# Kernel optimization log

Hardware: AMD Instinct MI355X
Metric: run time of the kernel (lower is better)

The kernel has to match this reference:

```python
import jax, jax.numpy as jnp
import numpy as np

D_MODEL = 768
NUM_HEADS = 12
HEAD_DIM = D_MODEL // NUM_HEADS


def setup_inputs() -> dict:
    key = jax.random.key(0)
    ks = jax.random.split(key, 9)
    B, S = 2, 2048
    s = 1.0 / np.sqrt(D_MODEL)
    x = jax.random.normal(ks[0], (B, S, D_MODEL), dtype=jnp.float32)
    Wq = jax.random.normal(ks[1], (D_MODEL, D_MODEL), dtype=jnp.float32) * s
    Wk = jax.random.normal(ks[2], (D_MODEL, D_MODEL), dtype=jnp.float32) * s
    Wv = jax.random.normal(ks[3], (D_MODEL, D_MODEL), dtype=jnp.float32) * s
    Wo = jax.random.normal(ks[4], (D_MODEL, D_MODEL), dtype=jnp.float32) * s
    bq = jax.random.normal(ks[5], (D_MODEL,), dtype=jnp.float32) * 0.01
    bk = jax.random.normal(ks[6], (D_MODEL,), dtype=jnp.float32) * 0.01
    bv = jax.random.normal(ks[7], (D_MODEL,), dtype=jnp.float32) * 0.01
    bo = jax.random.normal(ks[8], (D_MODEL,), dtype=jnp.float32) * 0.01
    return {"x": x, "Wq": Wq, "bq": bq, "Wk": Wk, "bk": bk,
            "Wv": Wv, "bv": bv, "Wo": Wo, "bo": bo}


def reference(x, Wq, bq, Wk, bk, Wv, bv, Wo, bo):
    B, S, _ = x.shape
    # projections; reshape to [B, H, S, Dh]
    def split_heads(t):
        return t.reshape(B, S, NUM_HEADS, HEAD_DIM).transpose(0, 2, 1, 3)
    q = split_heads(x @ Wq + bq)
    k = split_heads(x @ Wk + bk)
    v = split_heads(x @ Wv + bv)
    scale = 1.0 / np.sqrt(HEAD_DIM)
    scores = jnp.einsum("bhqd,bhkd->bhqk", q, k) * scale  # [B,H,S,S]
    attn = jax.nn.softmax(scores, axis=-1)
    # dropout p=0.0 (eval) -> identity
    ctx = jnp.einsum("bhqk,bhkd->bhqd", attn, v)
    ctx = ctx.transpose(0, 2, 1, 3).reshape(B, S, D_MODEL)
    return ctx @ Wo + bo
```

## Files before the change

kernel.cpp:

```cpp
#include <hip/hip_runtime.h>
#include <hip/hip_bf16.h>
#include <hip/hip_fp16.h>

#define D_MODEL 768
#define NHEADS  12
#define HD      64
#define BATCH   2
#define SEQ     2048
#define NTOK    (BATCH*SEQ)
#define NX      ((size_t)NTOK * D_MODEL)
#define NW      ((size_t)D_MODEL * D_MODEL)
#define NBH     (BATCH*NHEADS)
#define SC_LOG2 0.18033688f

typedef __attribute__((ext_vector_type(8))) short    short8;
typedef __attribute__((ext_vector_type(8))) _Float16 half8;
typedef __attribute__((ext_vector_type(2))) __fp16   fp16x2;
typedef __attribute__((ext_vector_type(4))) float    f32x4;

__device__ __forceinline__ float bf2f(short s) {
    union { unsigned u; float f; } c;
    c.u = ((unsigned)(unsigned short)s) << 16;
    return c.f;
}
__device__ __forceinline__ short f2bf(float f) {
    __hip_bfloat16 h = __float2bfloat16(f);
    return *(short*)&h;
}

#ifdef __has_builtin
#if __has_builtin(__builtin_amdgcn_global_load_lds)
#define HAS_GLD 1
#endif
#if __has_builtin(__builtin_amdgcn_exp2f)
#define EXP2(x) __builtin_amdgcn_exp2f(x)
#else
#define EXP2(x) exp2f(x)
#endif
#if __has_builtin(__builtin_amdgcn_cvt_pkrtz)
#define HAS_PKRTZ 1
#endif
#else
#define EXP2(x) exp2f(x)
#endif
#ifdef HAS_GLD
#define GLD16(gp, lp) __builtin_amdgcn_global_load_lds( \
    (const __attribute__((address_space(1))) void*)(gp), \
    (__attribute__((address_space(3))) void*)(lp), 16, 0, 0)
#endif

#ifdef HAS_PKRTZ
#define PKF16(a, b) __builtin_amdgcn_cvt_pkrtz((a), (b))
#else
#define PKF16(a, b) ((fp16x2){ (__fp16)(a), (__fp16)(b) })
#endif

__global__ __launch_bounds__(256) void fused_conv(
        const void* __restrict__ xin,
        const void* __restrict__ w0, const void* __restrict__ w1,
        const void* __restrict__ w2, const void* __restrict__ w3,
        const void* __restrict__ b0, const void* __restrict__ b1,
        const void* __restrict__ b2, const void* __restrict__ b3,
        short* __restrict__ xc, short* __restrict__ wt,
        short* __restrict__ bc, int* __restrict__ flag)
{
    __shared__ int red[256];
    __shared__ float T[64][65];
    const int tid = threadIdx.x;
    const int F = blockIdx.x;

    {
        const short* xs = (const short*)xin;
        int maxe = 0;
#pragma unroll
        for (int u = 0; u < 16; ++u) {
            int e = ((unsigned short)xs[tid * 16 + u] >> 7) & 0xFF;
            maxe = max(maxe, e);
        }
        red[tid] = maxe;
        __syncthreads();
        for (int s = 128; s > 0; s >>= 1) {
            if (tid < s) red[tid] = max(red[tid], red[tid + s]);
            __syncthreads();
        }
    }
    const bool isf = (red[0] > 140);

    if (F < 3072) {
        const int i = F * 256 + tid;
        if (isf) {
            float4 f = ((const float4*)xin)[i];
            short4 o = { f2bf(f.x), f2bf(f.y), f2bf(f.z), f2bf(f.w) };
            ((short4*)xc)[i] = o;
        } else {
            ((short4*)xc)[i] = ((const short4*)xin)[i];
        }
    } else if (F < 3648) {
        const int G = F - 3072;
        const int z = G / 144, rr = G % 144;
        const int k0 = (rr % 12) * 64, n0 = (rr / 12) * 64;
        const void* src = (z == 0) ? w0 : (z == 1) ? w1 : (z == 2) ? w2 : w3;
        const float sc = (z == 0) ? SC_LOG2 : 1.0f;
        const int la = tid & 15, lb = tid >> 4;
#pragma unroll
        for (int u = 0; u < 4; ++u) {
            const int kr = (lb & 3) + 4 * u + 16 * (lb >> 2);
            if (isf) {
                float4 f = *(const float4*)((const float*)src + (size_t)(k0 + kr) * D_MODEL + n0 + la * 4);
                T[kr][la*4+0] = f.x; T[kr][la*4+1] = f.y; T[kr][la*4+2] = f.z; T[kr][la*4+3] = f.w;
            } else {
                short4 s = *(const short4*)((const short*)src + (size_t)(k0 + kr) * D_MODEL + n0 + la * 4);
                T[kr][la*4+0] = bf2f(s.x); T[kr][la*4+1] = bf2f(s.y);
                T[kr][la*4+2] = bf2f(s.z); T[kr][la*4+3] = bf2f(s.w);
            }
        }
        __syncthreads();
#pragma unroll
        for (int u = 0; u < 4; ++u) {
            const int nr = (lb & 3) + 4 * u + 16 * (lb >> 2);
            short4 o = { f2bf(T[la*4+0][nr] * sc), f2bf(T[la*4+1][nr] * sc),
                         f2bf(T[la*4+2][nr] * sc), f2bf(T[la*4+3][nr] * sc) };
            *(short4*)(wt + (size_t)z * NW + (size_t)(n0 + nr) * D_MODEL + k0 + la * 4) = o;
        }
    } else {
        if (tid == 0) *flag = isf ? 1 : 0;
        const void* srcs[4] = { b0, b1, b2, b3 };
        for (int z = 0; z < 4; ++z) {
            const float sc = (z == 0) ? SC_LOG2 : 1.0f;
            for (int i = tid; i < D_MODEL; i += 256) {
                float v = isf ? ((const float*)srcs[z])[i] : bf2f(((const short*)srcs[z])[i]);
                bc[z * D_MODEL + i] = f2bf(v * sc);
            }
        }
    }
}

__global__ __launch_bounds__(512) void qkv_gemm(const short* __restrict__ X,
                                                const short* __restrict__ Wt,
                                                const short* __restrict__ bias,
                                                short* __restrict__ qb,
                                                short* __restrict__ kb,
                                                _Float16* __restrict__ Vt)
{
    __shared__ __align__(16) char shbuf[32768];
    short* Als = (short*)shbuf;
    short* Bls = (short*)(shbuf + 16384);
    _Float16* T = (_Float16*)shbuf;

    const int tid = threadIdx.x;
    const int wave = tid >> 6, lane = tid & 63;
    const int quad = lane >> 4, l16 = lane & 15;
    const int wm = wave & 3, wn = wave >> 2;
    const int m0 = blockIdx.x * 128;
    const int ng = blockIdx.y * 128;

    f32x4 acc[2][4];
#pragma unroll
    for (int nt = 0; nt < 4; ++nt) {
        const float bv = bf2f(bias[ng + wn*64 + nt*16 + l16]);
#pragma unroll
        for (int mt = 0; mt < 2; ++mt) acc[mt][nt] = (f32x4){bv, bv, bv, bv};
    }

    const int row = tid >> 2, ch = (tid & 3) * 8;
#ifdef HAS_GLD
#define QSTAGE(buf, k0) do { \
        GLD16(X  + (size_t)(m0 + row) * D_MODEL + (k0) + ch, &Als[(buf)*4096 + tid*8]); \
        GLD16(Wt + (size_t)(ng + row) * D_MODEL + (k0) + ch, &Bls[(buf)*4096 + tid*8]); \
    } while (0)
#else
#define QSTAGE(buf, k0) do { \
        short8 r0 = *(const short8*)(X  + (size_t)(m0 + row) * D_MODEL + (k0) + ch); \
        short8 r1 = *(const short8*)(Wt + (size_t)(ng + row) * D_MODEL + (k0) + ch); \
        *(short8*)&Als[(buf)*4096 + tid*8] = r0; \
        *(short8*)&Bls[(buf)*4096 + tid*8] = r1; \
    } while (0)
#endif

    QSTAGE(0, 0);
    __syncthreads();

    for (int ks = 0; ks < 24; ++ks) {
        const int cur = ks & 1;
        if (ks + 1 < 24) QSTAGE(cur ^ 1, (ks + 1) * 32);

        short8 a[2], b[4];
#pragma unroll
        for (int mt = 0; mt < 2; ++mt)
            a[mt] = *(const short8*)&Als[cur*4096 + (wm*32 + mt*16 + l16) * 32 + quad*8];
#pragma unroll
        for (int nt = 0; nt < 4; ++nt)
            b[nt] = *(const short8*)&Bls[cur*4096 + (wn*64 + nt*16 + l16) * 32 + quad*8];
#pragma unroll
        for (int mt = 0; mt < 2; ++mt)
#pragma unroll
        for (int nt = 0; nt < 4; ++nt)
            acc[mt][nt] = __builtin_amdgcn_mfma_f32_16x16x32_bf16(a[mt], b[nt], acc[mt][nt], 0, 0, 0);

        __syncthreads();
    }
#undef QSTAGE

    const int seg = blockIdx.y / 6;
    if (seg == 0) {
#pragma unroll
        for (int mt = 0; mt < 2; ++mt)
#pragma unroll
        for (int nt = 0; nt < 4; ++nt) {
            const int n = ng + wn*64 + nt*16 + l16;
#pragma unroll
            for (int r = 0; r < 4; ++r) {
                const int m = m0 + wm*32 + mt*16 + quad*4 + r;
                qb[(size_t)m * D_MODEL + n] = f2bf(acc[mt][nt][r]);
            }
        }
    } else if (seg == 1) {
        const int nl = ng - 768;
#pragma unroll
        for (int mt = 0; mt < 2; ++mt)
#pragma unroll
        for (int nt = 0; nt < 4; ++nt) {
            const int n = nl + wn*64 + nt*16 + l16;
            const int h = n >> 6, dh = n & 63;
            const int chunk = dh >> 3, dof = dh & 7;
#pragma unroll
            for (int r = 0; r < 4; ++r) {
                const int m = m0 + wm*32 + mt*16 + quad*4 + r;
                const int b2 = m >> 11, tok = m & (SEQ - 1);
                kb[((size_t)(b2*NHEADS + h)*32 + (tok >> 6))*4096
                   + chunk*512 + (tok & 63)*8 + dof] = f2bf(acc[mt][nt][r]);
            }
        }
    } else {
        const int batch = m0 >> 11, tokb0 = m0 & (SEQ - 1);
#pragma unroll
        for (int p = 0; p < 2; ++p) {
            if ((wm >> 1) == p) {
#pragma unroll
                for (int nt = 0; nt < 4; ++nt) {
                    const int dim_l = wn*64 + nt*16 + l16;
#pragma unroll
                    for (int mt = 0; mt < 2; ++mt) {
                        const int tok_l = (wm & 1)*32 + mt*16 + quad*4;
                        union { _Float16 h4[4]; int2 v; } u;
#pragma unroll
                        for (int r = 0; r < 4; ++r) u.h4[r] = (_Float16)acc[mt][nt][r];
                        *(int2*)&T[dim_l * 72 + tok_l] = u.v;
                    }
                }
            }
            __syncthreads();
#pragma unroll
            for (int u = 0; u < 2; ++u) {
                const int slot = tid + u * 512;
                const int drow = slot & 127, chk = slot >> 7;
                int4 val = *(const int4*)&T[drow * 72 + chk * 8];
                const int dim_g = ng - 1536 + drow;
                const int h = dim_g >> 6, dl = dim_g & 63;
                *(int4*)(Vt + ((size_t)((batch*NHEADS + h)*32) + (tokb0 >> 6) + p)*4096
                            + chk*512 + dl*8) = val;
            }
            if (p == 0) __syncthreads();
        }
    }
}

__global__ __launch_bounds__(256) void out_gemm(const _Float16* __restrict__ Op,
                                                const float* __restrict__ mlp,
                                                const short* __restrict__ Wt,
                                                const short* __restrict__ bias,
                                                void* __restrict__ outv,
                                                const int* __restrict__ flag)
{
    __shared__ short Als[2][2048];
    __shared__ short Bls[2][2048];

    const int tid = threadIdx.x;
    const int wave = tid >> 6, lane = tid & 63;
    const int quad = lane >> 4, l16 = lane & 15;
    const int m0 = blockIdx.x * 64;
    const int n0 = blockIdx.y * 64;

    f32x4 acc[4];
#pragma unroll
    for (int nt = 0; nt < 4; ++nt) {
        const float bv = bf2f(bias[n0 + nt*16 + l16]);
        acc[nt] = (f32x4){bv, bv, bv, bv};
    }

    const int row = tid >> 2, ch = (tid & 3) * 8;
    const int m = m0 + row;
    const int bhb = (m >> 11) * NHEADS;
    const int qq = m & (SEQ - 1);
    const _Float16* Op2 = Op + (size_t)(NBH * SEQ) * HD;

#define MLOAD(h) do { \
        const size_t r1 = (size_t)(bhb + (h)) * SEQ + qq; \
        const float2 ml1 = *(const float2*)&mlp[r1 * 2]; \
        const float2 ml2 = *(const float2*)&mlp[((size_t)(NBH * SEQ) + r1) * 2]; \
        const float M_ = fmaxf(ml1.x, ml2.x); \
        const float w1 = EXP2(ml1.x - M_) * ml1.y; \
        const float w2 = EXP2(ml2.x - M_) * ml2.y; \
        const float s_ = 1.0f / (w1 + w2); \
        f1 = w1 * s_; f2 = w2 * s_; \
    } while (0)

#define PLOAD(ks) do { \
        const int d = ((ks) & 1) * 32 + ch; \
        const size_t r1 = (size_t)(bhb + ((ks) >> 1)) * SEQ + qq; \
        p1 = *(const half8*)&Op[r1 * HD + d]; \
        p2 = *(const half8*)&Op2[r1 * HD + d]; \
    } while (0)

#define XSTORE(buf) do { \
        short8 xb; \
        _Pragma("unroll") \
        for (int j = 0; j < 8; ++j) \
            xb[j] = f2bf(f1 * (float)p1[j] + f2 * (float)p2[j]); \
        *(short8*)&Als[buf][tid*8] = xb; \
    } while (0)

#ifdef HAS_GLD
#define BSTAGE(buf, k0) \
        GLD16(Wt + (size_t)(n0 + row) * D_MODEL + (k0) + ch, &Bls[buf][tid*8])
#else
#define BSTAGE(buf, k0) do { \
        short8 r1_ = *(const short8*)(Wt + (size_t)(n0 + row) * D_MODEL + (k0) + ch); \
        *(short8*)&Bls[buf][tid*8] = r1_; } while (0)
#endif

    half8 p1, p2; float f1, f2;
    MLOAD(0); PLOAD(0); XSTORE(0);
    BSTAGE(0, 0);
    __syncthreads();

    for (int ks = 0; ks < 24; ++ks) {
        const int cur = ks & 1;
        if (ks + 1 < 24) {
            if (((ks + 1) & 1) == 0) MLOAD((ks + 1) >> 1);
            PLOAD(ks + 1);
            BSTAGE(cur ^ 1, (ks + 1) * 32);
        }

        short8 a = *(const short8*)&Als[cur][(wave*16 + l16) * 32 + quad*8];
#pragma unroll
        for (int nt = 0; nt < 4; ++nt) {
            short8 b = *(const short8*)&Bls[cur][(nt*16 + l16) * 32 + quad*8];
            acc[nt] = __builtin_amdgcn_mfma_f32_16x16x32_bf16(a, b, acc[nt], 0, 0, 0);
        }

        if (ks + 1 < 24) XSTORE(cur ^ 1);
        __syncthreads();
    }
#undef MLOAD
#undef PLOAD
#undef XSTORE
#undef BSTAGE

    const bool outf32 = (*flag != 0);
#pragma unroll
    for (int nt = 0; nt < 4; ++nt) {
        const int n = n0 + nt*16 + l16;
#pragma unroll
        for (int r = 0; r < 4; ++r) {
            const int mm = m0 + wave*16 + quad*4 + r;
            const size_t idx = (size_t)mm * D_MODEL + n;
            if (outf32) ((float*)outv)[idx] = acc[nt][r];
            else        ((short*)outv)[idx] = f2bf(acc[nt][r]);
        }
    }
}

__global__ __launch_bounds__(256, 3) void attn_mfma(const short* __restrict__ q,
                                                    const short* __restrict__ k,
                                                    const _Float16* __restrict__ Vt,
                                                    _Float16* __restrict__ Op,
                                                    float* __restrict__ mlp)
{
    __shared__ __align__(16) short    Kls[2][4096];
    __shared__ __align__(16) _Float16 Vls[2][4096];
    __shared__ __align__(16) _Float16 Pls[4][2048];

    const int tid  = threadIdx.x;
    const int wave = tid >> 6, lane = tid & 63;
    const int quad = lane >> 4, l16 = lane & 15;

    const int F = blockIdx.x;
    const int xcd = F & 7, slot = F >> 3;
    const int bh = xcd * 3 + (slot >> 5);
    const int rem = slot & 31;
    const int q0 = (rem >> 1) * 128;
    const int sp = rem & 1;
    const int b = bh / NHEADS, h = bh % NHEADS;
    const size_t bS = (size_t)b * SEQ;

    short8 qf[2][2];
#pragma unroll
    for (int col = 0; col < 2; ++col)
#pragma unroll
    for (int k0h = 0; k0h < 2; ++k0h)
        qf[col][k0h] = *(const short8*)(q + (bS + q0 + wave*32 + col*16 + l16) * D_MODEL
                                          + h*HD + k0h*32 + quad*8);

    half8 ones;
#pragma unroll
    for (int j = 0; j < 8; ++j) ones[j] = (_Float16)1.0f;

    const short*    kbase = k  + ((size_t)bh*32 + sp*16) * 4096;
    const _Float16* vbase = Vt + ((size_t)bh*32 + sp*16) * 4096;

#ifdef HAS_GLD
#define STAGE_K(buf, j0) do { \
        GLD16(kbase + (size_t)(j0)*64 + tid*8,       &Kls[buf][tid*8]); \
        GLD16(kbase + (size_t)(j0)*64 + (tid+256)*8, &Kls[buf][(tid+256)*8]); \
    } while (0)
#define STAGE_V(buf, j0) do { \
        GLD16(vbase + (size_t)(j0)*64 + tid*8,       &Vls[buf][tid*8]); \
        GLD16(vbase + (size_t)(j0)*64 + (tid+256)*8, &Vls[buf][(tid+256)*8]); \
    } while (0)
#else
#define STAGE_K(buf, j0) do { \
        short8 a_ = *(const short8*)(kbase + (size_t)(j0)*64 + tid*8); \
        short8 b_ = *(const short8*)(kbase + (size_t)(j0)*64 + (tid+256)*8); \
        *(short8*)&Kls[buf][tid*8] = a_;  *(short8*)&Kls[buf][(tid+256)*8] = b_; \
    } while (0)
#define STAGE_V(buf, j0) do { \
        half8 c_ = *(const half8*)(vbase + (size_t)(j0)*64 + tid*8); \
        half8 d_ = *(const half8*)(vbase + (size_t)(j0)*64 + (tid+256)*8); \
        *(half8*)&Vls[buf][tid*8] = c_;  *(half8*)&Vls[buf][(tid+256)*8] = d_; \
    } while (0)
#endif

    float m_ = -1e30f;
    f32x4 laccA = (f32x4){0.f,0.f,0.f,0.f}, laccB = (f32x4){0.f,0.f,0.f,0.f};
    f32x4 o[4][2];
#pragma unroll
    for (int t = 0; t < 4; ++t) { o[t][0] = (f32x4){0.f,0.f,0.f,0.f}; o[t][1] = (f32x4){0.f,0.f,0.f,0.f}; }

#define NT (SEQ / 2 / 64)

#define QK(S, KB) do { \
    _Pragma("unroll") \
    for (int t = 0; t < 4; ++t) { S[t][0] = (f32x4){0.f,0.f,0.f,0.f}; S[t][1] = (f32x4){0.f,0.f,0.f,0.f}; } \
    _Pragma("unroll") \
    for (int k0h = 0; k0h < 2; ++k0h) \
    _Pragma("unroll") \
    for (int t = 0; t < 4; ++t) { \
        short8 kf = *(const short8*)&Kls[KB][(k0h*4 + quad)*512 + (t*16 + l16)*8]; \
        S[t][0] = __builtin_amdgcn_mfma_f32_16x16x32_bf16(kf, qf[0][k0h], S[t][0], 0, 0, 0); \
        S[t][1] = __builtin_amdgcn_mfma_f32_16x16x32_bf16(kf, qf[1][k0h], S[t][1], 0, 0, 0); \
    } \
} while (0)

#define PV(VB) do { \
    _Pragma("unroll") \
    for (int k0h = 0; k0h < 2; ++k0h) { \
        half8 pf0 = *(half8*)&Pls[wave][(k0h*4 + quad)*128 + l16*8]; \
        half8 pf1 = *(half8*)&Pls[wave][1024 + (k0h*4 + quad)*128 + l16*8]; \
        laccA = __builtin_amdgcn_mfma_f32_16x16x32_f16(ones, pf0, laccA, 0, 0, 0); \
        laccB = __builtin_amdgcn_mfma_f32_16x16x32_f16(ones, pf1, laccB, 0, 0, 0); \
        _Pragma("unroll") \
        for (int t = 0; t < 4; ++t) { \
            half8 vf = *(const half8*)&Vls[VB][(k0h*4 + quad)*512 + (t*16 + l16)*8]; \
            o[t][0] = __builtin_amdgcn_mfma_f32_16x16x32_f16(vf, pf0, o[t][0], 0, 0, 0); \
            o[t][1] = __builtin_amdgcn_mfma_f32_16x16x32_f16(vf, pf1, o[t][1], 0, 0, 0); \
        } \
    } \
} while (0)

#define SOFTMAX(S) do { \
    float mx = S[0][0][0]; \
    _Pragma("unroll") \
    for (int t = 0; t < 4; ++t) \
    _Pragma("unroll") \
    for (int c = 0; c < 2; ++c) \
    _Pragma("unroll") \
    for (int r = 0; r < 4; ++r) mx = fmaxf(mx, S[t][c][r]); \
    if (__any(mx > m_ + 8.f)) { \
        _Pragma("unroll") \
        for (int d = 1; d < 64; d <<= 1) mx = fmaxf(mx, __shfl_xor(mx, d)); \
        const float mn = fmaxf(m_, mx); \
        const float al = EXP2(m_ - mn); \
        _Pragma("unroll") \
        for (int t = 0; t < 4; ++t) \
        _Pragma("unroll") \
        for (int c = 0; c < 2; ++c) { \
            o[t][c][0] *= al; o[t][c][1] *= al; o[t][c][2] *= al; o[t][c][3] *= al; \
        } \
        laccA[0] *= al; laccB[0] *= al; \
        m_ = mn; \
    } \
    _Pragma("unroll") \
    for (int t = 0; t < 4; ++t) \
    _Pragma("unroll") \
    for (int c = 0; c < 2; ++c) { \
        union { fp16x2 h2[2]; int2 v; } u4; \
        u4.h2[0] = PKF16(EXP2(S[t][c][0] - m_), EXP2(S[t][c][1] - m_)); \
        u4.h2[1] = PKF16(EXP2(S[t][c][2] - m_), EXP2(S[t][c][3] - m_)); \
        const int kc = 2*t + (quad >> 1); \
        *(int2*)&Pls[wave][c*1024 + kc*128 + l16*8 + (quad & 1)*4] = u4.v; \
    } \
} while (0)

#define BODY(JT) do { \
    if ((JT) + 2 < NT) STAGE_K(((JT) + 2) & 1, ((JT) + 2) * 64); \
    if ((JT) + 1 < NT) STAGE_V(((JT) + 1) & 1, ((JT) + 1) * 64); \
    f32x4 s_[4][2]; \
    __builtin_amdgcn_s_setprio(1); \
    if ((JT) + 1 < NT) QK(s_, ((JT) + 1) & 1); \
    PV((JT) & 1); \
    __builtin_amdgcn_s_setprio(0); \
    if ((JT) + 1 < NT) SOFTMAX(s_); \
    __syncthreads(); \
} while (0)

    STAGE_K(0, 0); STAGE_V(0, 0);
    __syncthreads();
    STAGE_K(1, 64);
    {
        f32x4 s_[4][2];
        QK(s_, 0);
        SOFTMAX(s_);
    }
    __syncthreads();

    for (int jt = 0; jt < NT; ++jt) BODY(jt);

#pragma unroll
    for (int col = 0; col < 2; ++col) {
        const f32x4 la = col ? laccB : laccA;
        const float inv = 1.0f / la[0];
        const int myq = q0 + wave*32 + col*16 + l16;
        const size_t prow = ((size_t)sp * (NBH * SEQ) + (size_t)bh * SEQ + myq);
        _Float16* orow = Op + prow * HD;
#pragma unroll
        for (int t = 0; t < 4; ++t) {
            union { _Float16 h4[4]; int2 v; } u4;
#pragma unroll
            for (int r = 0; r < 4; ++r) u4.h4[r] = (_Float16)(o[t][col][r] * inv);
            *(int2*)(orow + t*16 + quad*4) = u4.v;
        }
        if (quad == 0) {
            float2 mlv; mlv.x = m_; mlv.y = la[0];
            *(float2*)&mlp[prow * 2] = mlv;
        }
    }
#undef BODY
#undef SOFTMAX
#undef PV
#undef QK
#undef NT
#undef STAGE_K
#undef STAGE_V
}

extern "C" void kernel_launch(void* const* d_in, const int* in_sizes, int n_in,
                              void* d_out, int out_size, void* d_ws, size_t ws_size,
                              hipStream_t stream)
{
    int* flag = (int*)d_ws;
    short* xc = (short*)((char*)d_ws + 64);
    short* Wt = xc + NX;
    short* bc = Wt + 4 * NW;
    short* qb = bc + 4 * D_MODEL;
    short* kb = qb + NX;
    _Float16* Vt = (_Float16*)(kb + NX);
    _Float16* Op = (_Float16*)(Vt + NX);
    float* mlp = (float*)(Op + (size_t)2 * NBH * SEQ * HD);

    fused_conv<<<3649, 256, 0, stream>>>(d_in[0],
                                         d_in[1], d_in[3], d_in[5], d_in[7],
                                         d_in[2], d_in[4], d_in[6], d_in[8],
                                         xc, Wt, bc, flag);

    qkv_gemm<<<dim3(NTOK/128, 2304/128), 512, 0, stream>>>(xc, Wt, bc, qb, kb, Vt);

    attn_mfma<<<768, 256, 0, stream>>>(qb, kb, Vt, Op, mlp);

    out_gemm<<<dim3(NTOK/64, D_MODEL/64), 256, 0, stream>>>(Op, mlp, Wt + 3*NW, bc + 3*D_MODEL, d_out, flag);
}
```

Measured before the change: 169.1 us.

## Split attention keys four ways and read K/V fragments directly from global

Raises the key-dimension split from 2 to 4, doubling the attention grid and raising the occupancy hint, and extends the combine step in the output GEMM to merge four partial results. It also drops the LDS double-buffered K/V staging and its per-tile barriers, loading MFMA fragments straight from global memory into registers. This aims to improve CU utilisation and remove sync overhead, but it exposes global-load latency in the inner loop and doubles the partial-output traffic and combine work.

New measurement: 195.1 us. 15.4% more time.

```diff
diff --git a/kernel.cpp b/kernel.cpp
--- a/kernel.cpp
+++ b/kernel.cpp
@@ -11,6 +11,7 @@
 #define NX      ((size_t)NTOK * D_MODEL)
 #define NW      ((size_t)D_MODEL * D_MODEL)
 #define NBH     (BATCH*NHEADS)
+#define NSPLIT  4
 #define SC_LOG2 0.18033688f
 
 typedef __attribute__((ext_vector_type(8))) short    short8;
@@ -292,31 +293,39 @@
     const int m = m0 + row;
     const int bhb = (m >> 11) * NHEADS;
     const int qq = m & (SEQ - 1);
-    const _Float16* Op2 = Op + (size_t)(NBH * SEQ) * HD;
 
 #define MLOAD(h) do { \
         const size_t r1 = (size_t)(bhb + (h)) * SEQ + qq; \
-        const float2 ml1 = *(const float2*)&mlp[r1 * 2]; \
-        const float2 ml2 = *(const float2*)&mlp[((size_t)(NBH * SEQ) + r1) * 2]; \
-        const float M_ = fmaxf(ml1.x, ml2.x); \
-        const float w1 = EXP2(ml1.x - M_) * ml1.y; \
-        const float w2 = EXP2(ml2.x - M_) * ml2.y; \
-        const float s_ = 1.0f / (w1 + w2); \
-        f1 = w1 * s_; f2 = w2 * s_; \
+        float2 ml[NSPLIT]; float M_ = -1e30f; \
+        _Pragma("unroll") \
+        for (int s = 0; s < NSPLIT; ++s) { \
+            ml[s] = *(const float2*)&mlp[((size_t)s * (NBH * SEQ) + r1) * 2]; \
+            M_ = fmaxf(M_, ml[s].x); \
+        } \
+        float w[NSPLIT]; float tot = 0.f; \
+        _Pragma("unroll") \
+        for (int s = 0; s < NSPLIT; ++s) { w[s] = EXP2(ml[s].x - M_) * ml[s].y; tot += w[s]; } \
+        const float inv_ = 1.0f / tot; \
+        _Pragma("unroll") \
+        for (int s = 0; s < NSPLIT; ++s) fw[s] = w[s] * inv_; \
     } while (0)
 
 #define PLOAD(ks) do { \
         const int d = ((ks) & 1) * 32 + ch; \
         const size_t r1 = (size_t)(bhb + ((ks) >> 1)) * SEQ + qq; \
-        p1 = *(const half8*)&Op[r1 * HD + d]; \
-        p2 = *(const half8*)&Op2[r1 * HD + d]; \
+        _Pragma("unroll") \
+        for (int s = 0; s < NSPLIT; ++s) \
+            p[s] = *(const half8*)&Op[((size_t)s * (NBH * SEQ) + r1) * HD + d]; \
     } while (0)
 
 #define XSTORE(buf) do { \
         short8 xb; \
         _Pragma("unroll") \
-        for (int j = 0; j < 8; ++j) \
-            xb[j] = f2bf(f1 * (float)p1[j] + f2 * (float)p2[j]); \
+        for (int j = 0; j < 8; ++j) { \
+            float v_ = fw[0] * (float)p[0][j] + fw[1] * (float)p[1][j] \
+                     + fw[2] * (float)p[2][j] + fw[3] * (float)p[3][j]; \
+            xb[j] = f2bf(v_); \
+        } \
         *(short8*)&Als[buf][tid*8] = xb; \
     } while (0)
 
@@ -329,7 +338,7 @@
         *(short8*)&Bls[buf][tid*8] = r1_; } while (0)
 #endif
 
-    half8 p1, p2; float f1, f2;
+    half8 p[NSPLIT]; float fw[NSPLIT];
     MLOAD(0); PLOAD(0); XSTORE(0);
     BSTAGE(0, 0);
     __syncthreads();
@@ -371,14 +380,12 @@
     }
 }
 
-__global__ __launch_bounds__(256, 3) void attn_mfma(const short* __restrict__ q,
+__global__ __launch_bounds__(256, 4) void attn_mfma(const short* __restrict__ q,
                                                     const short* __restrict__ k,
                                                     const _Float16* __restrict__ Vt,
                                                     _Float16* __restrict__ Op,
                                                     float* __restrict__ mlp)
 {
-    __shared__ __align__(16) short    Kls[2][4096];
-    __shared__ __align__(16) _Float16 Vls[2][4096];
     __shared__ __align__(16) _Float16 Pls[4][2048];
 
     const int tid  = threadIdx.x;
@@ -387,10 +394,10 @@
 
     const int F = blockIdx.x;
     const int xcd = F & 7, slot = F >> 3;
-    const int bh = xcd * 3 + (slot >> 5);
-    const int rem = slot & 31;
-    const int q0 = (rem >> 1) * 128;
-    const int sp = rem & 1;
+    const int bh = xcd * 3 + (slot >> 6);
+    const int rem = slot & 63;
+    const int q0 = (rem >> 2) * 128;
+    const int sp = rem & 3;
     const int b = bh / NHEADS, h = bh % NHEADS;
     const size_t bS = (size_t)b * SEQ;
 
@@ -406,30 +413,8 @@
 #pragma unroll
     for (int j = 0; j < 8; ++j) ones[j] = (_Float16)1.0f;
 
-    const short*    kbase = k  + ((size_t)bh*32 + sp*16) * 4096;
-    const _Float16* vbase = Vt + ((size_t)bh*32 + sp*16) * 4096;
-
-#ifdef HAS_GLD
-#define STAGE_K(buf, j0) do { \
-        GLD16(kbase + (size_t)(j0)*64 + tid*8,       &Kls[buf][tid*8]); \
-        GLD16(kbase + (size_t)(j0)*64 + (tid+256)*8, &Kls[buf][(tid+256)*8]); \
-    } while (0)
-#define STAGE_V(buf, j0) do { \
-        GLD16(vbase + (size_t)(j0)*64 + tid*8,       &Vls[buf][tid*8]); \
-        GLD16(vbase + (size_t)(j0)*64 + (tid+256)*8, &Vls[buf][(tid+256)*8]); \
-    } while (0)
-#else
-#define STAGE_K(buf, j0) do { \
-        short8 a_ = *(const short8*)(kbase + (size_t)(j0)*64 + tid*8); \
-        short8 b_ = *(const short8*)(kbase + (size_t)(j0)*64 + (tid+256)*8); \
-        *(short8*)&Kls[buf][tid*8] = a_;  *(short8*)&Kls[buf][(tid+256)*8] = b_; \
-    } while (0)
-#define STAGE_V(buf, j0) do { \
-        half8 c_ = *(const half8*)(vbase + (size_t)(j0)*64 + tid*8); \
-        half8 d_ = *(const half8*)(vbase + (size_t)(j0)*64 + (tid+256)*8); \
-        *(half8*)&Vls[buf][tid*8] = c_;  *(half8*)&Vls[buf][(tid+256)*8] = d_; \
-    } while (0)
-#endif
+    const short*    kT = k  + ((size_t)bh*32 + sp*8) * 4096 + quad*512 + l16*8;
+    const _Float16* vT = Vt + ((size_t)bh*32 + sp*8) * 4096 + quad*512 + l16*8;
 
     float m_ = -1e30f;
     f32x4 laccA = (f32x4){0.f,0.f,0.f,0.f}, laccB = (f32x4){0.f,0.f,0.f,0.f};
@@ -437,94 +422,78 @@
 #pragma unroll
     for (int t = 0; t < 4; ++t) { o[t][0] = (f32x4){0.f,0.f,0.f,0.f}; o[t][1] = (f32x4){0.f,0.f,0.f,0.f}; }
 
-#define NT (SEQ / 2 / 64)
-
-#define QK(S, KB) do { \
-    _Pragma("unroll") \
-    for (int t = 0; t < 4; ++t) { S[t][0] = (f32x4){0.f,0.f,0.f,0.f}; S[t][1] = (f32x4){0.f,0.f,0.f,0.f}; } \
-    _Pragma("unroll") \
-    for (int k0h = 0; k0h < 2; ++k0h) \
-    _Pragma("unroll") \
-    for (int t = 0; t < 4; ++t) { \
-        short8 kf = *(const short8*)&Kls[KB][(k0h*4 + quad)*512 + (t*16 + l16)*8]; \
-        S[t][0] = __builtin_amdgcn_mfma_f32_16x16x32_bf16(kf, qf[0][k0h], S[t][0], 0, 0, 0); \
-        S[t][1] = __builtin_amdgcn_mfma_f32_16x16x32_bf16(kf, qf[1][k0h], S[t][1], 0, 0, 0); \
-    } \
-} while (0)
-
-#define PV(VB) do { \
-    _Pragma("unroll") \
-    for (int k0h = 0; k0h < 2; ++k0h) { \
-        half8 pf0 = *(half8*)&Pls[wave][(k0h*4 + quad)*128 + l16*8]; \
-        half8 pf1 = *(half8*)&Pls[wave][1024 + (k0h*4 + quad)*128 + l16*8]; \
-        laccA = __builtin_amdgcn_mfma_f32_16x16x32_f16(ones, pf0, laccA, 0, 0, 0); \
-        laccB = __builtin_amdgcn_mfma_f32_16x16x32_f16(ones, pf1, laccB, 0, 0, 0); \
-        _Pragma("unroll") \
-        for (int t = 0; t < 4; ++t) { \
-            half8 vf = *(const half8*)&Vls[VB][(k0h*4 + quad)*512 + (t*16 + l16)*8]; \
-            o[t][0] = __builtin_amdgcn_mfma_f32_16x16x32_f16(vf, pf0, o[t][0], 0, 0, 0); \
-            o[t][1] = __builtin_amdgcn_mfma_f32_16x16x32_f16(vf, pf1, o[t][1], 0, 0, 0); \
-        } \
-    } \
-} while (0)
-
-#define SOFTMAX(S) do { \
-    float mx = S[0][0][0]; \
-    _Pragma("unroll") \
-    for (int t = 0; t < 4; ++t) \
-    _Pragma("unroll") \
-    for (int c = 0; c < 2; ++c) \
-    _Pragma("unroll") \
-    for (int r = 0; r < 4; ++r) mx = fmaxf(mx, S[t][c][r]); \
-    if (__any(mx > m_ + 8.f)) { \
-        _Pragma("unroll") \
-        for (int d = 1; d < 64; d <<= 1) mx = fmaxf(mx, __shfl_xor(mx, d)); \
-        const float mn = fmaxf(m_, mx); \
-        const float al = EXP2(m_ - mn); \
-        _Pragma("unroll") \
-        for (int t = 0; t < 4; ++t) \
-        _Pragma("unroll") \
-        for (int c = 0; c < 2; ++c) { \
-            o[t][c][0] *= al; o[t][c][1] *= al; o[t][c][2] *= al; o[t][c][3] *= al; \
-        } \
-        laccA[0] *= al; laccB[0] *= al; \
-        m_ = mn; \
-    } \
-    _Pragma("unroll") \
-    for (int t = 0; t < 4; ++t) \
-    _Pragma("unroll") \
-    for (int c = 0; c < 2; ++c) { \
-        union { fp16x2 h2[2]; int2 v; } u4; \
-        u4.h2[0] = PKF16(EXP2(S[t][c][0] - m_), EXP2(S[t][c][1] - m_)); \
-        u4.h2[1] = PKF16(EXP2(S[t][c][2] - m_), EXP2(S[t][c][3] - m_)); \
-        const int kc = 2*t + (quad >> 1); \
-        *(int2*)&Pls[wave][c*1024 + kc*128 + l16*8 + (quad & 1)*4] = u4.v; \
-    } \
-} while (0)
-
-#define BODY(JT) do { \
-    if ((JT) + 2 < NT) STAGE_K(((JT) + 2) & 1, ((JT) + 2) * 64); \
-    if ((JT) + 1 < NT) STAGE_V(((JT) + 1) & 1, ((JT) + 1) * 64); \
-    f32x4 s_[4][2]; \
-    __builtin_amdgcn_s_setprio(1); \
-    if ((JT) + 1 < NT) QK(s_, ((JT) + 1) & 1); \
-    PV((JT) & 1); \
-    __builtin_amdgcn_s_setprio(0); \
-    if ((JT) + 1 < NT) SOFTMAX(s_); \
-    __syncthreads(); \
-} while (0)
-
-    STAGE_K(0, 0); STAGE_V(0, 0);
-    __syncthreads();
-    STAGE_K(1, 64);
-    {
+#define NT 8
+
+#pragma unroll 2
+    for (int jt = 0; jt < NT; ++jt) {
+        const short*    kj = kT + (size_t)jt * 4096;
+        const _Float16* vj = vT + (size_t)jt * 4096;
+
         f32x4 s_[4][2];
-        QK(s_, 0);
-        SOFTMAX(s_);
-    }
-    __syncthreads();
-
-    for (int jt = 0; jt < NT; ++jt) BODY(jt);
+#pragma unroll
+        for (int t = 0; t < 4; ++t) { s_[t][0] = (f32x4){0.f,0.f,0.f,0.f}; s_[t][1] = (f32x4){0.f,0.f,0.f,0.f}; }
+        __builtin_amdgcn_s_setprio(1);
+#pragma unroll
+        for (int k0h = 0; k0h < 2; ++k0h)
+#pragma unroll
+        for (int t = 0; t < 4; ++t) {
+            short8 kf = *(const short8*)(kj + k0h*2048 + t*128);
+            s_[t][0] = __builtin_amdgcn_mfma_f32_16x16x32_bf16(kf, qf[0][k0h], s_[t][0], 0, 0, 0);
+            s_[t][1] = __builtin_amdgcn_mfma_f32_16x16x32_bf16(kf, qf[1][k0h], s_[t][1], 0, 0, 0);
+        }
+        __builtin_amdgcn_s_setprio(0);
+
+        {
+            float mx = s_[0][0][0];
+#pragma unroll
+            for (int t = 0; t < 4; ++t)
+#pragma unroll
+            for (int c = 0; c < 2; ++c)
+#pragma unroll
+            for (int r = 0; r < 4; ++r) mx = fmaxf(mx, s_[t][c][r]);
+            if (__any(mx > m_ + 8.f)) {
+#pragma unroll
+                for (int d = 1; d < 64; d <<= 1) mx = fmaxf(mx, __shfl_xor(mx, d));
+                const float mn = fmaxf(m_, mx);
+                const float al = EXP2(m_ - mn);
+#pragma unroll
+                for (int t = 0; t < 4; ++t)
+#pragma unroll
+                for (int c = 0; c < 2; ++c) {
+                    o[t][c][0] *= al; o[t][c][1] *= al; o[t][c][2] *= al; o[t][c][3] *= al;
+                }
+                laccA[0] *= al; laccB[0] *= al;
+                m_ = mn;
+            }
+#pragma unroll
+            for (int t = 0; t < 4; ++t)
+#pragma unroll
+            for (int c = 0; c < 2; ++c) {
+                union { fp16x2 h2[2]; int2 v; } u4;
+                u4.h2[0] = PKF16(EXP2(s_[t][c][0] - m_), EXP2(s_[t][c][1] - m_));
+                u4.h2[1] = PKF16(EXP2(s_[t][c][2] - m_), EXP2(s_[t][c][3] - m_));
+                const int kc = 2*t + (quad >> 1);
+                *(int2*)&Pls[wave][c*1024 + kc*128 + l16*8 + (quad & 1)*4] = u4.v;
+            }
+        }
+
+        __builtin_amdgcn_s_setprio(1);
+#pragma unroll
+        for (int k0h = 0; k0h < 2; ++k0h) {
+            half8 pf0 = *(half8*)&Pls[wave][(k0h*4 + quad)*128 + l16*8];
+            half8 pf1 = *(half8*)&Pls[wave][1024 + (k0h*4 + quad)*128 + l16*8];
+            laccA = __builtin_amdgcn_mfma_f32_16x16x32_f16(ones, pf0, laccA, 0, 0, 0);
+            laccB = __builtin_amdgcn_mfma_f32_16x16x32_f16(ones, pf1, laccB, 0, 0, 0);
+#pragma unroll
+            for (int t = 0; t < 4; ++t) {
+                half8 vf = *(const half8*)(vj + k0h*2048 + t*128);
+                o[t][0] = __builtin_amdgcn_mfma_f32_16x16x32_f16(vf, pf0, o[t][0], 0, 0, 0);
+                o[t][1] = __builtin_amdgcn_mfma_f32_16x16x32_f16(vf, pf1, o[t][1], 0, 0, 0);
+            }
+        }
+        __builtin_amdgcn_s_setprio(0);
+    }
+#undef NT
 
 #pragma unroll
     for (int col = 0; col < 2; ++col) {
@@ -545,13 +514,6 @@
             *(float2*)&mlp[prow * 2] = mlv;
         }
     }
-#undef BODY
-#undef SOFTMAX
-#undef PV
-#undef QK
-#undef NT
-#undef STAGE_K
-#undef STAGE_V
 }
 
 extern "C" void kernel_launch(void* const* d_in, const int* in_sizes, int n_in,
@@ -566,7 +528,7 @@
     short* kb = qb + NX;
     _Float16* Vt = (_Float16*)(kb + NX);
     _Float16* Op = (_Float16*)(Vt + NX);
-    float* mlp = (float*)(Op + (size_t)2 * NBH * SEQ * HD);
+    float* mlp = (float*)(Op + (size_t)NSPLIT * NBH * SEQ * HD);
 
     fused_conv<<<3649, 256, 0, stream>>>(d_in[0],
                                          d_in[1], d_in[3], d_in[5], d_in[7],
@@ -575,7 +537,7 @@
 
     qkv_gemm<<<dim3(NTOK/128, 2304/128), 512, 0, stream>>>(xc, Wt, bc, qb, kb, Vt);
 
-    attn_mfma<<<768, 256, 0, stream>>>(qb, kb, Vt, Op, mlp);
+    attn_mfma<<<1536, 256, 0, stream>>>(qb, kb, Vt, Op, mlp);
 
     out_gemm<<<dim3(NTOK/64, D_MODEL/64), 256, 0, stream>>>(Op, mlp, Wt + 3*NW, bc + 3*D_MODEL, d_out, flag);
 }
```
